# Optimization experiments

Measured on AMD Instinct MI355X. Metric: run time of the kernel, lower is better.

The kernel has to match this reference:

```python
import jax, jax.numpy as jnp
import numpy as np

N_NODES = 50000
N_EDGES = 400000


def _gcn_norm(edge_index, num_nodes):
    """Add self-loops and compute symmetric GCN normalization coefficients.

    Returns (src, dst, norm) where out[dst] += norm * h[src].
    """
    loop = jnp.arange(num_nodes, dtype=edge_index.dtype)
    src = jnp.concatenate([edge_index[0], loop])
    dst = jnp.concatenate([edge_index[1], loop])
    ones = jnp.ones(src.shape[0], dtype=jnp.float32)
    deg = jax.ops.segment_sum(ones, dst, num_segments=num_nodes)
    d_inv_sqrt = jnp.where(deg > 0, jax.lax.rsqrt(jnp.maximum(deg, 1.0)), 0.0)
    norm = d_inv_sqrt[src] * d_inv_sqrt[dst]
    return src, dst, norm


def _gcn_conv(x, W, b, src, dst, norm, num_nodes):
    h = x @ W                              # [N, out] dense GEMM first (PyG GCNConv order)
    msg = h[src] * norm[:, None]           # [E+N, out] gather + scale
    agg = jax.ops.segment_sum(msg, dst, num_segments=num_nodes)  # scatter-add
    return agg + b


def setup_inputs() -> dict:
    key = jax.random.key(0)
    k1, k2, k3, k4, k5, k6 = jax.random.split(key, 6)
    x = jax.random.normal(k1, (N_NODES, 128), dtype=jnp.float32)
    edge_index = jax.random.randint(k2, (2, N_EDGES), 0, N_NODES, dtype=jnp.int64)
    # Glorot-ish scaled params
    W1 = jax.random.normal(k3, (128, 512), dtype=jnp.float32) * (1.0 / np.sqrt(128))
    b1 = jnp.zeros((512,), dtype=jnp.float32)
    W2 = jax.random.normal(k4, (512, 250), dtype=jnp.float32) * (1.0 / np.sqrt(512))
    b2 = jnp.zeros((250,), dtype=jnp.float32)
    return {"x": x, "edge_index": edge_index, "W1": W1, "b1": b1, "W2": W2, "b2": b2}


def reference(x, edge_index, W1, b1, W2, b2):
    num_nodes = x.shape[0]
    src, dst, norm = _gcn_norm(edge_index, num_nodes)
    h = _gcn_conv(x, W1, b1, src, dst, norm, num_nodes)
    h = jax.nn.relu(h)
    h = _gcn_conv(h, W2, b2, src, dst, norm, num_nodes)
    return jax.nn.relu(h)
```

## Files before the change

kernel.cpp:

```cpp
#include <hip/hip_runtime.h>

constexpr int NN  = 50000;
constexpr int NE  = 400000;
constexpr int F0  = 128;
constexpr int F1  = 512;
constexpr int F2  = 250;
constexpr int MT32 = 1563;
constexpr int SLOT = 64;

typedef short  short8 __attribute__((ext_vector_type(8)));
typedef float  f32x4  __attribute__((ext_vector_type(4)));

__device__ inline unsigned short f2bf(float f) {
    union { float f; unsigned u; } v; v.f = f;
    unsigned u = v.u;
    return (unsigned short)((u + 0x7FFFu + ((u >> 16) & 1u)) >> 16);
}
__device__ inline float bf2f(unsigned short h) {
    union { unsigned u; float f; } v; v.u = ((unsigned)h) << 16;
    return v.f;
}
__device__ inline float bflo(unsigned u) {
    union { unsigned u; float f; } v; v.u = u << 16; return v.f;
}
__device__ inline float bfhi(unsigned u) {
    union { unsigned u; float f; } v; v.u = u & 0xFFFF0000u; return v.f;
}

__global__ void k_build(const int4* __restrict__ src4, const int4* __restrict__ dst4,
                        int* __restrict__ cnt, int* __restrict__ slot) {
    int t = blockIdx.x * 256 + threadIdx.x;
    if (t >= NE / 4) return;
    int4 s = src4[t];
    int4 d = dst4[t];
    int p;
    p = atomicAdd(&cnt[d.x], 1); if (p < SLOT) slot[d.x * SLOT + p] = s.x;
    p = atomicAdd(&cnt[d.y], 1); if (p < SLOT) slot[d.y * SLOT + p] = s.y;
    p = atomicAdd(&cnt[d.z], 1); if (p < SLOT) slot[d.z * SLOT + p] = s.z;
    p = atomicAdd(&cnt[d.w], 1); if (p < SLOT) slot[d.w * SLOT + p] = s.w;
}

__global__ __launch_bounds__(256) void k_prep(
        const float4* __restrict__ x4, const int* __restrict__ cnt,
        ushort4* __restrict__ xs,
        const float* __restrict__ W1, unsigned short* __restrict__ w1t,
        const float* __restrict__ W2, unsigned short* __restrict__ w2t) {
    int b = blockIdx.x;
    if (b < 6250) {
        int t = b * 256 + threadIdx.x;
        float dn = rsqrtf((float)cnt[t >> 5] + 1.0f);
        float4 v = x4[t];
        ushort4 o;
        o.x = f2bf(dn * v.x); o.y = f2bf(dn * v.y);
        o.z = f2bf(dn * v.z); o.w = f2bf(dn * v.w);
        xs[t] = o;
    } else if (b < 6250 + 256) {
        int t = (b - 6250) * 256 + threadIdx.x;
        int n = t >> 7, k = t & 127;
        w1t[t] = f2bf(W1[k * F1 + n]);
    } else {
        int t = (b - 6506) * 256 + threadIdx.x;
        int n = t >> 9, k = t & 511;
        w2t[t] = (n < F2) ? f2bf(W2[k * F2 + n]) : (unsigned short)0;
    }
}

__global__ __launch_bounds__(256) void k_gather1(
        const unsigned int* __restrict__ xs, const int* __restrict__ slot,
        const int* __restrict__ cnt, unsigned int* __restrict__ agg) {
    int n = blockIdx.x * 4 + (threadIdx.x >> 6);
    int c = threadIdx.x & 63;
    if (n >= NN) return;
    int deg = cnt[n]; if (deg > SLOT) deg = SLOT;
    float dn = rsqrtf((float)deg + 1.0f);
    const int* sl = slot + n * SLOT;
    unsigned a = xs[(size_t)n * 64 + c];
    float s0 = bflo(a), s1 = bfhi(a);
    int j = 0;
    for (; j + 8 <= deg; j += 8) {
        int i0 = sl[j],     i1 = sl[j + 1], i2 = sl[j + 2], i3 = sl[j + 3];
        int i4 = sl[j + 4], i5 = sl[j + 5], i6 = sl[j + 6], i7 = sl[j + 7];
        unsigned v0 = xs[(size_t)i0 * 64 + c];
        unsigned v1 = xs[(size_t)i1 * 64 + c];
        unsigned v2 = xs[(size_t)i2 * 64 + c];
        unsigned v3 = xs[(size_t)i3 * 64 + c];
        unsigned v4 = xs[(size_t)i4 * 64 + c];
        unsigned v5 = xs[(size_t)i5 * 64 + c];
        unsigned v6 = xs[(size_t)i6 * 64 + c];
        unsigned v7 = xs[(size_t)i7 * 64 + c];
        s0 += bflo(v0) + bflo(v1) + bflo(v2) + bflo(v3)
            + bflo(v4) + bflo(v5) + bflo(v6) + bflo(v7);
        s1 += bfhi(v0) + bfhi(v1) + bfhi(v2) + bfhi(v3)
            + bfhi(v4) + bfhi(v5) + bfhi(v6) + bfhi(v7);
    }
    for (; j + 4 <= deg; j += 4) {
        int i0 = sl[j], i1 = sl[j + 1], i2 = sl[j + 2], i3 = sl[j + 3];
        unsigned v0 = xs[(size_t)i0 * 64 + c];
        unsigned v1 = xs[(size_t)i1 * 64 + c];
        unsigned v2 = xs[(size_t)i2 * 64 + c];
        unsigned v3 = xs[(size_t)i3 * 64 + c];
        s0 += bflo(v0) + bflo(v1) + bflo(v2) + bflo(v3);
        s1 += bfhi(v0) + bfhi(v1) + bfhi(v2) + bfhi(v3);
    }
    for (; j < deg; ++j) {
        unsigned v = xs[(size_t)sl[j] * 64 + c];
        s0 += bflo(v); s1 += bfhi(v);
    }
    agg[(size_t)n * 64 + c] =
        (unsigned)f2bf(dn * s0) | ((unsigned)f2bf(dn * s1) << 16);
}

__global__ __launch_bounds__(256) void k_fused(
        const unsigned short* __restrict__ A,
        const unsigned short* __restrict__ W1t,
        const unsigned short* __restrict__ W2t,
        const float* __restrict__ b1,
        const int* __restrict__ cnt,
        unsigned short* __restrict__ C,
        int M)
{
    __shared__ unsigned short Bs[2][64 * 128];
    __shared__ unsigned short H[32 * 512];

    const int tid = threadIdx.x;
    const int wv = tid >> 6, ln = tid & 63;
    const int wy = wv >> 1, wx = wv & 1;
    const int lane15 = ln & 15, quad = ln >> 4;
    const int m0 = blockIdx.x * 32;

    int arow = m0 + wy * 16 + lane15; if (arow > M - 1) arow = M - 1;
    const short8* ap = (const short8*)(A + (size_t)arow * 128);
    short8 af4[4];
#pragma unroll
    for (int kk = 0; kk < 4; ++kk) af4[kk] = ap[kk * 4 + quad];

#pragma unroll
    for (int i = 0; i < 4; ++i) {
        int c = i * 256 + tid;
        int n = c >> 4, q = c & 15;
        int gq = q ^ (n & 15);
        __builtin_amdgcn_global_load_lds(
            (const __attribute__((address_space(1))) void*)(W1t + (size_t)n * 128 + gq * 8),
            (__attribute__((address_space(3))) void*)(&Bs[0][0] + (i * 4 + wv) * 512), 16, 0, 0);
    }

    for (int it = 0; it < 8; ++it) {
        __syncthreads();
        if (it < 7) {
            int n0n = (it + 1) * 64;
#pragma unroll
            for (int i = 0; i < 4; ++i) {
                int c = i * 256 + tid;
                int n = c >> 4, q = c & 15;
                int gq = q ^ (n & 15);
                __builtin_amdgcn_global_load_lds(
                    (const __attribute__((address_space(1))) void*)(W1t + (size_t)(n0n + n) * 128 + gq * 8),
                    (__attribute__((address_space(3))) void*)(&Bs[(it + 1) & 1][0] + (i * 4 + wv) * 512), 16, 0, 0);
            }
        } else {
#pragma unroll
            for (int i = 0; i < 4; ++i) {
                int c = i * 256 + tid;
                int n = c >> 2, q = c & 3;
                int gq = q ^ ((n >> 1) & 3);
                __builtin_amdgcn_global_load_lds(
                    (const __attribute__((address_space(1))) void*)(W2t + (size_t)n * 512 + gq * 8),
                    (__attribute__((address_space(3))) void*)(&Bs[0][0] + (i * 4 + wv) * 512), 16, 0, 0);
            }
        }
        const unsigned short* B = &Bs[it & 1][0];
        f32x4 acc[2];
        acc[0] = (f32x4)0.0f; acc[1] = (f32x4)0.0f;
#pragma unroll
        for (int kk = 0; kk < 4; ++kk) {
            short8 bf[2];
#pragma unroll
            for (int f = 0; f < 2; ++f) {
                int nB = wx * 32 + f * 16 + lane15;
                int sB = (kk * 4 + quad) ^ (nB & 15);
                bf[f] = *(const short8*)(B + nB * 128 + sB * 8);
            }
#pragma unroll
            for (int f = 0; f < 2; ++f)
                acc[f] = __builtin_amdgcn_mfma_f32_16x16x32_bf16(
                    af4[kk], bf[f], acc[f], 0, 0, 0);
        }
#pragma unroll
        for (int f = 0; f < 2; ++f) {
            int col = it * 64 + wx * 32 + f * 16 + lane15;
            float bia = b1[col];
#pragma unroll
            for (int r = 0; r < 4; ++r) {
                int lrow = wy * 16 + quad * 4 + r;
                unsigned byteoff = (unsigned)(lrow * 1024 + col * 2)
                                 ^ (unsigned)((lrow & 7) << 4);
                *(unsigned short*)((char*)H + byteoff) =
                    f2bf(fmaxf(acc[f][r] + bia, 0.0f));
            }
        }
    }

    const unsigned hbase = (unsigned)((wy * 16 + lane15) * 1024);
    const unsigned hxor  = (unsigned)(((wy * 16 + lane15) & 7) << 4);

    f32x4 acc2[8];
#pragma unroll
    for (int f = 0; f < 8; ++f) acc2[f] = (f32x4)0.0f;

    for (int ks = 0; ks < 16; ++ks) {
        __syncthreads();
        if (ks < 15) {
            int ko = (ks + 1) << 5;
#pragma unroll
            for (int i = 0; i < 4; ++i) {
                int c = i * 256 + tid;
                int n = c >> 2, q = c & 3;
                int gq = q ^ ((n >> 1) & 3);
                __builtin_amdgcn_global_load_lds(
                    (const __attribute__((address_space(1))) void*)(W2t + (size_t)n * 512 + ko + gq * 8),
                    (__attribute__((address_space(3))) void*)(&Bs[(ks + 1) & 1][0] + (i * 4 + wv) * 512), 16, 0, 0);
            }
        }
        const unsigned short* B = &Bs[ks & 1][0];
        short8 afv = *(const short8*)((const char*)H
                        + ((hbase + (unsigned)(ks * 64 + quad * 16)) ^ hxor));
        short8 bf[8];
#pragma unroll
        for (int f = 0; f < 8; ++f) {
            int nB = wx * 128 + f * 16 + lane15;
            int sB = quad ^ ((nB >> 1) & 3);
            bf[f] = *(const short8*)(B + nB * 32 + sB * 8);
        }
#pragma unroll
        for (int f = 0; f < 8; ++f)
            acc2[f] = __builtin_amdgcn_mfma_f32_16x16x32_bf16(
                afv, bf[f], acc2[f], 0, 0, 0);
    }

    float rs[4];
#pragma unroll
    for (int r = 0; r < 4; ++r) {
        int row = m0 + wy * 16 + quad * 4 + r; if (row > M - 1) row = M - 1;
        rs[r] = rsqrtf((float)cnt[row] + 1.0f);
    }
#pragma unroll
    for (int f = 0; f < 8; ++f) {
        int col = wx * 128 + f * 16 + lane15;
        f32x4 v = acc2[f];
#pragma unroll
        for (int r = 0; r < 4; ++r) {
            int row = m0 + wy * 16 + quad * 4 + r;
            if (row < M)
                C[(size_t)row * 256 + col] = f2bf(v[r] * rs[r]);
        }
    }
}

__global__ __launch_bounds__(256) void k_gather2(
        const ushort4* __restrict__ t4, const int* __restrict__ slot,
        const int* __restrict__ cnt, const float* __restrict__ b2,
        float* __restrict__ out) {
    int n = blockIdx.x * 4 + (threadIdx.x >> 6);
    int c = threadIdx.x & 63;
    if (n >= NN) return;
    int deg = cnt[n]; if (deg > SLOT) deg = SLOT;
    float dn = rsqrtf((float)deg + 1.0f);
    const int* sl = slot + n * SLOT;
    ushort4 a = t4[(size_t)n * 64 + c];
    float sx = bf2f(a.x), sy = bf2f(a.y), sz = bf2f(a.z), sw = bf2f(a.w);
    int j = 0;
    for (; j + 8 <= deg; j += 8) {
        int i0 = sl[j],     i1 = sl[j + 1], i2 = sl[j + 2], i3 = sl[j + 3];
        int i4 = sl[j + 4], i5 = sl[j + 5], i6 = sl[j + 6], i7 = sl[j + 7];
        ushort4 v0 = t4[(size_t)i0 * 64 + c];
        ushort4 v1 = t4[(size_t)i1 * 64 + c];
        ushort4 v2 = t4[(size_t)i2 * 64 + c];
        ushort4 v3 = t4[(size_t)i3 * 64 + c];
        ushort4 v4 = t4[(size_t)i4 * 64 + c];
        ushort4 v5 = t4[(size_t)i5 * 64 + c];
        ushort4 v6 = t4[(size_t)i6 * 64 + c];
        ushort4 v7 = t4[(size_t)i7 * 64 + c];
        sx += bf2f(v0.x) + bf2f(v1.x) + bf2f(v2.x) + bf2f(v3.x)
            + bf2f(v4.x) + bf2f(v5.x) + bf2f(v6.x) + bf2f(v7.x);
        sy += bf2f(v0.y) + bf2f(v1.y) + bf2f(v2.y) + bf2f(v3.y)
            + bf2f(v4.y) + bf2f(v5.y) + bf2f(v6.y) + bf2f(v7.y);
        sz += bf2f(v0.z) + bf2f(v1.z) + bf2f(v2.z) + bf2f(v3.z)
            + bf2f(v4.z) + bf2f(v5.z) + bf2f(v6.z) + bf2f(v7.z);
        sw += bf2f(v0.w) + bf2f(v1.w) + bf2f(v2.w) + bf2f(v3.w)
            + bf2f(v4.w) + bf2f(v5.w) + bf2f(v6.w) + bf2f(v7.w);
    }
    for (; j + 4 <= deg; j += 4) {
        int i0 = sl[j], i1 = sl[j + 1], i2 = sl[j + 2], i3 = sl[j + 3];
        ushort4 v0 = t4[(size_t)i0 * 64 + c];
        ushort4 v1 = t4[(size_t)i1 * 64 + c];
        ushort4 v2 = t4[(size_t)i2 * 64 + c];
        ushort4 v3 = t4[(size_t)i3 * 64 + c];
        sx += bf2f(v0.x) + bf2f(v1.x) + bf2f(v2.x) + bf2f(v3.x);
        sy += bf2f(v0.y) + bf2f(v1.y) + bf2f(v2.y) + bf2f(v3.y);
        sz += bf2f(v0.z) + bf2f(v1.z) + bf2f(v2.z) + bf2f(v3.z);
        sw += bf2f(v0.w) + bf2f(v1.w) + bf2f(v2.w) + bf2f(v3.w);
    }
    for (; j < deg; ++j) {
        ushort4 v = t4[(size_t)sl[j] * 64 + c];
        sx += bf2f(v.x); sy += bf2f(v.y); sz += bf2f(v.z); sw += bf2f(v.w);
    }
    int f = c * 4;
    float* o = out + (size_t)n * F2;
    if (f     < F2) o[f]     = fmaxf(dn * sx + b2[f],     0.f);
    if (f + 1 < F2) o[f + 1] = fmaxf(dn * sy + b2[f + 1], 0.f);
    if (f + 2 < F2) o[f + 2] = fmaxf(dn * sz + b2[f + 2], 0.f);
    if (f + 3 < F2) o[f + 3] = fmaxf(dn * sw + b2[f + 3], 0.f);
}

extern "C" void kernel_launch(void* const* d_in, const int* in_sizes, int n_in,
                              void* d_out, int out_size, void* d_ws, size_t ws_size,
                              hipStream_t stream) {
    const float* x  = (const float*)d_in[0];
    const int*   ei = (const int*)d_in[1];
    const float* W1 = (const float*)d_in[2];
    const float* b1 = (const float*)d_in[3];
    const float* W2 = (const float*)d_in[4];
    const float* b2 = (const float*)d_in[5];
    float* out = (float*)d_out;

    char* p = (char*)d_ws;
    auto carve = [&](size_t bytes) { char* r = p; p += (bytes + 255) & ~(size_t)255; return r; };
    int*            cnt  = (int*)carve(NN * 4);
    int*            slot = (int*)carve((size_t)NN * SLOT * 4);
    unsigned short* xs   = (unsigned short*)carve((size_t)NN * F0 * 2);
    unsigned short* agg1 = (unsigned short*)carve((size_t)NN * F0 * 2);
    unsigned short* t2s  = (unsigned short*)carve((size_t)NN * 256 * 2);
    unsigned short* w1t  = (unsigned short*)carve((size_t)F1 * F0 * 2);
    unsigned short* w2t  = (unsigned short*)carve((size_t)256 * F1 * 2);

    hipMemsetAsync(cnt, 0, NN * sizeof(int), stream);
    k_build<<<(NE / 4 + 255) / 256, 256, 0, stream>>>(
        (const int4*)ei, (const int4*)(ei + NE), cnt, slot);
    k_prep<<<6250 + 256 + 512, 256, 0, stream>>>(
        (const float4*)x, cnt, (ushort4*)xs, W1, w1t, W2, w2t);
    k_gather1<<<(NN + 3) / 4, 256, 0, stream>>>((const unsigned int*)xs, slot, cnt,
                                                (unsigned int*)agg1);
    k_fused<<<MT32, 256, 0, stream>>>(agg1, w1t, w2t, b1, cnt, t2s, NN);
    k_gather2<<<(NN + 3) / 4, 256, 0, stream>>>((const ushort4*)t2s, slot, cnt, b2, out);
}
```

Baseline: 239.7 us.

## Retile fused GCN GEMM to 64-row blocks with direct-global weight fragments

The fused two-layer GEMM kernel now processes 64 rows per block instead of 32. Each wave owns a column strip of the output and reuses four row fragments per weight fragment. The double-buffered LDS staging of W1/W2 and its per-iteration barriers are removed, and weight fragments are loaded straight from global memory (L2-resident) into registers. This cuts block count and sync overhead and raises MFMA work per weight load, at the cost of more registers, more LDS for H (64 KB), and possible lower occupancy or uncoalesced global weight reads.

```diff
diff --git a/kernel.cpp b/kernel.cpp
--- a/kernel.cpp
+++ b/kernel.cpp
@@ -5,7 +5,7 @@
 constexpr int F0  = 128;
 constexpr int F1  = 512;
 constexpr int F2  = 250;
-constexpr int MT32 = 1563;
+constexpr int MT64 = 782;
 constexpr int SLOT = 64;
 
 typedef short  short8 __attribute__((ext_vector_type(8)));
@@ -119,139 +119,103 @@
         unsigned short* __restrict__ C,
         int M)
 {
-    __shared__ unsigned short Bs[2][64 * 128];
-    __shared__ unsigned short H[32 * 512];
+    __shared__ unsigned short H[64 * 512];
 
     const int tid = threadIdx.x;
     const int wv = tid >> 6, ln = tid & 63;
-    const int wy = wv >> 1, wx = wv & 1;
     const int lane15 = ln & 15, quad = ln >> 4;
-    const int m0 = blockIdx.x * 32;
-
-    int arow = m0 + wy * 16 + lane15; if (arow > M - 1) arow = M - 1;
-    const short8* ap = (const short8*)(A + (size_t)arow * 128);
-    short8 af4[4];
-#pragma unroll
-    for (int kk = 0; kk < 4; ++kk) af4[kk] = ap[kk * 4 + quad];
-
-#pragma unroll
-    for (int i = 0; i < 4; ++i) {
-        int c = i * 256 + tid;
-        int n = c >> 4, q = c & 15;
-        int gq = q ^ (n & 15);
-        __builtin_amdgcn_global_load_lds(
-            (const __attribute__((address_space(1))) void*)(W1t + (size_t)n * 128 + gq * 8),
-            (__attribute__((address_space(3))) void*)(&Bs[0][0] + (i * 4 + wv) * 512), 16, 0, 0);
-    }
-
-    for (int it = 0; it < 8; ++it) {
-        __syncthreads();
-        if (it < 7) {
-            int n0n = (it + 1) * 64;
-#pragma unroll
-            for (int i = 0; i < 4; ++i) {
-                int c = i * 256 + tid;
-                int n = c >> 4, q = c & 15;
-                int gq = q ^ (n & 15);
-                __builtin_amdgcn_global_load_lds(
-                    (const __attribute__((address_space(1))) void*)(W1t + (size_t)(n0n + n) * 128 + gq * 8),
-                    (__attribute__((address_space(3))) void*)(&Bs[(it + 1) & 1][0] + (i * 4 + wv) * 512), 16, 0, 0);
-            }
-        } else {
-#pragma unroll
-            for (int i = 0; i < 4; ++i) {
-                int c = i * 256 + tid;
-                int n = c >> 2, q = c & 3;
-                int gq = q ^ ((n >> 1) & 3);
-                __builtin_amdgcn_global_load_lds(
-                    (const __attribute__((address_space(1))) void*)(W2t + (size_t)n * 512 + gq * 8),
-                    (__attribute__((address_space(3))) void*)(&Bs[0][0] + (i * 4 + wv) * 512), 16, 0, 0);
-            }
-        }
-        const unsigned short* B = &Bs[it & 1][0];
-        f32x4 acc[2];
-        acc[0] = (f32x4)0.0f; acc[1] = (f32x4)0.0f;
-#pragma unroll
-        for (int kk = 0; kk < 4; ++kk) {
-            short8 bf[2];
-#pragma unroll
-            for (int f = 0; f < 2; ++f) {
-                int nB = wx * 32 + f * 16 + lane15;
-                int sB = (kk * 4 + quad) ^ (nB & 15);
-                bf[f] = *(const short8*)(B + nB * 128 + sB * 8);
-            }
-#pragma unroll
-            for (int f = 0; f < 2; ++f)
-                acc[f] = __builtin_amdgcn_mfma_f32_16x16x32_bf16(
-                    af4[kk], bf[f], acc[f], 0, 0, 0);
-        }
-#pragma unroll
-        for (int f = 0; f < 2; ++f) {
-            int col = it * 64 + wx * 32 + f * 16 + lane15;
-            float bia = b1[col];
+    const int m0 = blockIdx.x * 64;
+
+    short8 af[4][4];
+#pragma unroll
+    for (int rf = 0; rf < 4; ++rf) {
+        int arow = m0 + rf * 16 + lane15; if (arow > M - 1) arow = M - 1;
+        const short8* ap = (const short8*)(A + (size_t)arow * 128);
+#pragma unroll
+        for (int kk = 0; kk < 4; ++kk)
+            af[rf][kk] = ap[kk * 4 + quad];
+    }
+
+#pragma unroll 2
+    for (int f = 0; f < 8; ++f) {
+        const int nB = wv * 128 + f * 16 + lane15;
+        const short8* bp = (const short8*)(W1t + (size_t)nB * 128);
+        short8 bf[4];
+#pragma unroll
+        for (int kk = 0; kk < 4; ++kk) bf[kk] = bp[kk * 4 + quad];
+        f32x4 acc[4];
+#pragma unroll
+        for (int rf = 0; rf < 4; ++rf) acc[rf] = (f32x4)0.0f;
+#pragma unroll
+        for (int kk = 0; kk < 4; ++kk)
+#pragma unroll
+            for (int rf = 0; rf < 4; ++rf)
+                acc[rf] = __builtin_amdgcn_mfma_f32_16x16x32_bf16(
+                    af[rf][kk], bf[kk], acc[rf], 0, 0, 0);
+        const float bia = b1[nB];
+#pragma unroll
+        for (int rf = 0; rf < 4; ++rf)
 #pragma unroll
             for (int r = 0; r < 4; ++r) {
-                int lrow = wy * 16 + quad * 4 + r;
-                unsigned byteoff = (unsigned)(lrow * 1024 + col * 2)
+                int lrow = rf * 16 + quad * 4 + r;
+                unsigned byteoff = (unsigned)(lrow * 1024 + nB * 2)
                                  ^ (unsigned)((lrow & 7) << 4);
                 *(unsigned short*)((char*)H + byteoff) =
-                    f2bf(fmaxf(acc[f][r] + bia, 0.0f));
+                    f2bf(fmaxf(acc[rf][r] + bia, 0.0f));
             }
+    }
+
+    __syncthreads();
+
+    f32x4 acc2[4][4];
+#pragma unroll
+    for (int rf = 0; rf < 4; ++rf)
+#pragma unroll
+        for (int cf = 0; cf < 4; ++cf)
+            acc2[rf][cf] = (f32x4)0.0f;
+
+#pragma unroll 2
+    for (int ks = 0; ks < 16; ++ks) {
+        short8 bf[4];
+#pragma unroll
+        for (int cf = 0; cf < 4; ++cf) {
+            int nB = wv * 64 + cf * 16 + lane15;
+            bf[cf] = *(const short8*)(W2t + (size_t)nB * 512 + ks * 32 + quad * 8);
         }
-    }
-
-    const unsigned hbase = (unsigned)((wy * 16 + lane15) * 1024);
-    const unsigned hxor  = (unsigned)(((wy * 16 + lane15) & 7) << 4);
-
-    f32x4 acc2[8];
-#pragma unroll
-    for (int f = 0; f < 8; ++f) acc2[f] = (f32x4)0.0f;
-
-    for (int ks = 0; ks < 16; ++ks) {
-        __syncthreads();
-        if (ks < 15) {
-            int ko = (ks + 1) << 5;
-#pragma unroll
-            for (int i = 0; i < 4; ++i) {
-                int c = i * 256 + tid;
-                int n = c >> 2, q = c & 3;
-                int gq = q ^ ((n >> 1) & 3);
-                __builtin_amdgcn_global_load_lds(
-                    (const __attribute__((address_space(1))) void*)(W2t + (size_t)n * 512 + ko + gq * 8),
-                    (__attribute__((address_space(3))) void*)(&Bs[(ks + 1) & 1][0] + (i * 4 + wv) * 512), 16, 0, 0);
+        short8 hf[4];
+#pragma unroll
+        for (int rf = 0; rf < 4; ++rf) {
+            int lrow = rf * 16 + lane15;
+            unsigned byteoff = (unsigned)(lrow * 1024 + (ks * 32 + quad * 8) * 2)
+                             ^ (unsigned)((lrow & 7) << 4);
+            hf[rf] = *(const short8*)((const char*)H + byteoff);
+        }
+#pragma unroll
+        for (int rf = 0; rf < 4; ++rf)
+#pragma unroll
+            for (int cf = 0; cf < 4; ++cf)
+                acc2[rf][cf] = __builtin_amdgcn_mfma_f32_16x16x32_bf16(
+                    hf[rf], bf[cf], acc2[rf][cf], 0, 0, 0);
+    }
+
+#pragma unroll
+    for (int rf = 0; rf < 4; ++rf) {
+        float rs[4];
+#pragma unroll
+        for (int r = 0; r < 4; ++r) {
+            int row = m0 + rf * 16 + quad * 4 + r; if (row > M - 1) row = M - 1;
+            rs[r] = rsqrtf((float)cnt[row] + 1.0f);
+        }
+#pragma unroll
+        for (int cf = 0; cf < 4; ++cf) {
+            int col = wv * 64 + cf * 16 + lane15;
+            f32x4 v = acc2[rf][cf];
+#pragma unroll
+            for (int r = 0; r < 4; ++r) {
+                int row = m0 + rf * 16 + quad * 4 + r;
+                if (row < M)
+                    C[(size_t)row * 256 + col] = f2bf(v[r] * rs[r]);
             }
-        }
-        const unsigned short* B = &Bs[ks & 1][0];
-        short8 afv = *(const short8*)((const char*)H
-                        + ((hbase + (unsigned)(ks * 64 + quad * 16)) ^ hxor));
-        short8 bf[8];
-#pragma unroll
-        for (int f = 0; f < 8; ++f) {
-            int nB = wx * 128 + f * 16 + lane15;
-            int sB = quad ^ ((nB >> 1) & 3);
-            bf[f] = *(const short8*)(B + nB * 32 + sB * 8);
-        }
-#pragma unroll
-        for (int f = 0; f < 8; ++f)
-            acc2[f] = __builtin_amdgcn_mfma_f32_16x16x32_bf16(
-                afv, bf[f], acc2[f], 0, 0, 0);
-    }
-
-    float rs[4];
-#pragma unroll
-    for (int r = 0; r < 4; ++r) {
-        int row = m0 + wy * 16 + quad * 4 + r; if (row > M - 1) row = M - 1;
-        rs[r] = rsqrtf((float)cnt[row] + 1.0f);
-    }
-#pragma unroll
-    for (int f = 0; f < 8; ++f) {
-        int col = wx * 128 + f * 16 + lane15;
-        f32x4 v = acc2[f];
-#pragma unroll
-        for (int r = 0; r < 4; ++r) {
-            int row = m0 + wy * 16 + quad * 4 + r;
-            if (row < M)
-                C[(size_t)row * 256 + col] = f2bf(v[r] * rs[r]);
         }
     }
 }
@@ -340,6 +304,6 @@
         (const float4*)x, cnt, (ushort4*)xs, W1, w1t, W2, w2t);
     k_gather1<<<(NN + 3) / 4, 256, 0, stream>>>((const unsigned int*)xs, slot, cnt,
                                                 (unsigned int*)agg1);
-    k_fused<<<MT32, 256, 0, stream>>>(agg1, w1t, w2t, b1, cnt, t2s, NN);
+    k_fused<<<MT64, 256, 0, stream>>>(agg1, w1t, w2t, b1, cnt, t2s, NN);
     k_gather2<<<(NN + 3) / 4, 256, 0, stream>>>((const ushort4*)t2s, slot, cnt, b2, out);
 }
```

After: 237.4 us. About the same (-1.0%).
